# Kernel optimization log

Hardware: AMD Instinct MI355X
Metric: run time of the kernel (lower is better)

Reference implementation:

```python
import jax, jax.numpy as jnp
import numpy as np

B, S, D, H, DH = 2, 4096, 768, 12, 64

def setup_inputs() -> dict:
    key = jax.random.key(0)
    kx, kq, kk, kv = jax.random.split(key, 4)
    x = jax.random.normal(kx, (B, S, D), dtype=jnp.float32)
    # per-head Q/K/V projection weights, stacked over heads: [H, d_in, d_out]
    Wq = jax.random.normal(kq, (H, D, DH), dtype=jnp.float32) * 0.02
    Wk = jax.random.normal(kk, (H, D, DH), dtype=jnp.float32) * 0.02
    Wv = jax.random.normal(kv, (H, D, DH), dtype=jnp.float32) * 0.02
    return {"x": x, "Wq": Wq, "Wk": Wk, "Wv": Wv}

def reference(x, Wq, Wk, Wv):
    b, s, _ = x.shape
    # per-head linear projections (qkv_bias=False), batched over heads
    q = jnp.einsum('bsd,hde->bhse', x, Wq)  # [B,H,S,DH]
    k = jnp.einsum('bsd,hde->bhse', x, Wk)
    v = jnp.einsum('bsd,hde->bhse', x, Wv)
    scale = 1.0 / jnp.sqrt(jnp.asarray(q.shape[-1], q.dtype))
    scores = jnp.einsum('bhqe,bhke->bhqk', q, k) * scale  # [B,H,S,S]
    causal_mask = jnp.triu(jnp.ones((s, s), dtype=bool), k=1)
    scores = jnp.where(causal_mask, -jnp.inf, scores)
    attn = jax.nn.softmax(scores, axis=-1)  # dropout p=0 -> identity
    ctx = jnp.einsum('bhqk,bhke->bhqe', attn, v)  # [B,H,S,DH]
    # concat heads on last dim (matches torch.cat of per-head outputs)
    return ctx.transpose(0, 2, 1, 3).reshape(b, s, -1)  # [B,S,H*DH]
```

## Files before the change

### kernel.cpp

```cpp
#include <hip/hip_runtime.h>
#include <hip/hip_bf16.h>
#include <stdint.h>

#define B_  2
#define S_  4096
#define D_  768
#define H_  12
#define DH_ 64
#define BS_ (B_*S_)

typedef __bf16 bf16x8 __attribute__((ext_vector_type(8)));
typedef short  svec8  __attribute__((ext_vector_type(8)));
typedef float  fvec4  __attribute__((ext_vector_type(4)));
typedef int    ivec4  __attribute__((ext_vector_type(4)));
typedef unsigned short ushort_t;

__device__ __forceinline__ ushort_t bfc(float f){
    return __builtin_bit_cast(ushort_t, (__bf16)f);
}

__device__ __forceinline__ unsigned cvt_pk_bf16(float lo, float hi){
    unsigned r;
    asm("v_cvt_pk_bf16_f32 %0, %1, %2" : "=v"(r) : "v"(lo), "v"(hi));
    return r;
}

__device__ __forceinline__ fvec4 mfma16(svec8 a, svec8 b, fvec4 c){
    return __builtin_amdgcn_mfma_f32_16x16x32_bf16(
        __builtin_bit_cast(bf16x8, a), __builtin_bit_cast(bf16x8, b), c, 0, 0, 0);
}

__global__ __launch_bounds__(256) void prep(
    const float* __restrict__ X,
    const float* __restrict__ Wq, const float* __restrict__ Wk, const float* __restrict__ Wv,
    ushort_t* __restrict__ Xb, ushort_t* __restrict__ Wsz)
{
    const int bid = blockIdx.x;
    if (bid < 3072) {
        size_t idx = ((size_t)bid * 256 + threadIdx.x) * 8;
        float4 d0 = *(const float4*)(X + idx);
        float4 d1 = *(const float4*)(X + idx + 4);
        bf16x8 pk;
        pk[0] = (__bf16)d0.x; pk[1] = (__bf16)d0.y;
        pk[2] = (__bf16)d0.z; pk[3] = (__bf16)d0.w;
        pk[4] = (__bf16)d1.x; pk[5] = (__bf16)d1.y;
        pk[6] = (__bf16)d1.z; pk[7] = (__bf16)d1.w;
        *(svec8*)(Xb + idx) = __builtin_bit_cast(svec8, pk);
    } else {
        const int v  = bid - 3072;
        const int wt = v % 3;
        const int hk = v / 3;
        const int h  = hk / 12, kt = hk % 12;
        const float* W  = (wt == 0) ? Wq : (wt == 1) ? Wk : Wv;
        const float* Wh = W + (size_t)h * (D_ * DH_) + (size_t)kt * 64 * DH_;
        ushort_t* dst = Wsz + (size_t)(hk * 3 + wt) * 4096;
        #pragma unroll
        for (int i = 0; i < 16; i++) {
            int idx = threadIdx.x * 16 + i;
            int k = idx >> 6, n = idx & 63;
            float val = Wh[k * DH_ + n];
            int addr = (((k >> 5) * 4 + (n >> 4)) * 64 + (n & 15) * 4 + ((k >> 3) & 3)) * 8
                     + (k & 7);
            dst[addr] = bfc(val);
        }
    }
}

__global__ __launch_bounds__(256, 3) void qkv_proj(
    const ushort_t* __restrict__ Xb, const ushort_t* __restrict__ Wsz,
    ushort_t* __restrict__ Qb, ushort_t* __restrict__ Kb, ushort_t* __restrict__ Vg)
{
    const int m0 = blockIdx.x * 128;
    const int h  = blockIdx.y;

    __shared__ ushort_t smem[128 * 64 + 3 * 4096];
    ushort_t* Xs  = smem;
    ushort_t* Wts = smem + 128 * 64;
    ushort_t* XsT = smem;

    const int tid  = threadIdx.x;
    const int w    = tid >> 6;
    const int lane = tid & 63;
    const int quad = lane >> 4;
    const int l15  = lane & 15;
    const int lp8  = (l15 * 4 + quad) * 8;

    fvec4 acc[3][2][4];
    #pragma unroll
    for (int wt = 0; wt < 3; wt++)
        #pragma unroll
        for (int i = 0; i < 2; i++)
            #pragma unroll
            for (int j = 0; j < 4; j++) acc[wt][i][j] = (fvec4){0.f, 0.f, 0.f, 0.f};

    const ushort_t* xsrc = Xb + (size_t)m0 * D_;
    const ushort_t* wsrc = Wsz + (size_t)(h * 12) * 3 * 4096;

    int xr[4], xdu[4];
    #pragma unroll
    for (int i = 0; i < 4; i++) {
        int v = tid + 256 * i;
        int r = v >> 3, t = v & 7;
        xr[i]  = r * D_ + t * 8;
        xdu[i] = (((r >> 4) * 2 + (t >> 2)) * 64 + (r & 15) * 4 + (t & 3)) * 8;
    }

    svec8 xd[4];
    #pragma unroll
    for (int i = 0; i < 4; i++) xd[i] = *(const svec8*)(xsrc + xr[i]);

    for (int kt = 0; kt < 12; kt++) {
        const ushort_t* wp = wsrc + (size_t)kt * 3 * 4096;
        svec8 wd[6];
        #pragma unroll
        for (int j = 0; j < 6; j++)
            wd[j] = *(const svec8*)(wp + (tid + 256 * j) * 8);
        #pragma unroll
        for (int i = 0; i < 4; i++) *(svec8*)(Xs + xdu[i]) = xd[i];
        #pragma unroll
        for (int j = 0; j < 6; j++) *(svec8*)(Wts + (tid + 256 * j) * 8) = wd[j];
        __syncthreads();

        if (kt < 11) {
            #pragma unroll
            for (int i = 0; i < 4; i++)
                xd[i] = *(const svec8*)(xsrc + xr[i] + (kt + 1) * 64);
        }

        #pragma unroll
        for (int ks = 0; ks < 2; ks++) {
            svec8 a0 = *(const svec8*)(Xs + (4 * w + ks) * 512 + lp8);
            svec8 a1 = *(const svec8*)(Xs + (4 * w + 2 + ks) * 512 + lp8);
            #pragma unroll
            for (int wt = 0; wt < 3; wt++)
                #pragma unroll
                for (int ns = 0; ns < 4; ns++) {
                    svec8 b = *(const svec8*)(Wts + (wt * 8 + ks * 4 + ns) * 512 + lp8);
                    acc[wt][0][ns] = mfma16(a0, b, acc[wt][0][ns]);
                    acc[wt][1][ns] = mfma16(a1, b, acc[wt][1][ns]);
                }
        }
        __syncthreads();
    }

    const float qs = 0.18033688011112042f;
    #pragma unroll
    for (int ms = 0; ms < 2; ms++)
        #pragma unroll
        for (int ns = 0; ns < 4; ns++)
            #pragma unroll
            for (int r = 0; r < 4; r++) {
                int row = m0 + 32 * w + ms * 16 + quad * 4 + r;
                int col = h * DH_ + ns * 16 + l15;
                Qb[(size_t)row * D_ + col] = bfc(acc[0][ms][ns][r] * qs);
                Kb[(size_t)row * D_ + col] = bfc(acc[1][ms][ns][r]);
            }
    #pragma unroll
    for (int ms = 0; ms < 2; ms++)
        #pragma unroll
        for (int ns = 0; ns < 4; ns++)
            #pragma unroll
            for (int r = 0; r < 4; r++) {
                int sl = 32 * w + ms * 16 + quad * 4 + r;
                int e  = ns * 16 + l15;
                XsT[e * 136 + sl] = bfc(acc[2][ms][ns][r]);
            }
    __syncthreads();
    #pragma unroll
    for (int i = 0; i < 4; i++) {
        int v = tid + 256 * i;
        int e = v >> 4, s0 = (v & 15) * 8;
        svec8 d = *(const svec8*)(XsT + e * 136 + s0);
        *(svec8*)(Vg + (size_t)(h * DH_ + e) * BS_ + m0 + s0) = d;
    }
}

__global__ __launch_bounds__(256, 5) void attn(
    const ushort_t* __restrict__ Qb, const ushort_t* __restrict__ Kb,
    const ushort_t* __restrict__ Vg, float* __restrict__ Out)
{
    const int fid = blockIdx.x;
    const int qt  = (S_ / 64 - 1) - fid / (H_ * B_);
    const int r24 = fid % (H_ * B_);
    const int h   = r24 % H_;
    const int b   = r24 / H_;
    const int q0 = qt * 64;

    const int tid  = threadIdx.x;
    const int w    = tid >> 6;
    const int lane = tid & 63;
    const int quad = lane >> 4;
    const int l15  = lane & 15;

    __shared__ ushort_t Ks[64 * 72];
    __shared__ ushort_t Vt[64 * 72];

    const size_t hb = (size_t)b * S_ * D_ + (size_t)h * DH_;
    const ushort_t* Vh = Vg + (size_t)h * DH_ * BS_ + (size_t)b * S_;

    const int sr = tid >> 3;
    const int sc = (tid & 7) * 8;
    const int pr0 = (((sr      >> 2) & 1) << 5) | (((sr      >> 5) & 1) << 4) |
                    (((sr      >> 4) & 1) << 3) | (((sr      >> 3) & 1) << 2) | (sr & 3);
    const int sr1 = sr + 32;
    const int pr1 = (((sr1 >> 2) & 1) << 5) | (((sr1 >> 5) & 1) << 4) |
                    (((sr1 >> 4) & 1) << 3) | (((sr1 >> 3) & 1) << 2) | (sr1 & 3);

    svec8 aq[2];
    {
        const ushort_t* qrow = Qb + hb + (size_t)(q0 + 16 * w + l15) * D_;
        aq[0] = *(const svec8*)(qrow + quad * 8);
        aq[1] = *(const svec8*)(qrow + 32 + quad * 8);
    }

    float m_i = -INFINITY;
    float ls  = 0.f;
    fvec4 acc[4];
    #pragma unroll
    for (int n = 0; n < 4; n++) acc[n] = (fvec4){0.f, 0.f, 0.f, 0.f};

    const ushort_t* kp = Kb + hb + (size_t)sr * D_ + sc;
    const ushort_t* vp = Vh + (size_t)sr * BS_ + sc;

    svec8 kd[2], vd[2];
    kd[0] = *(const svec8*)(kp);
    kd[1] = *(const svec8*)(kp + (size_t)32 * D_);
    vd[0] = *(const svec8*)(vp);
    vd[1] = *(const svec8*)(vp + (size_t)32 * BS_);
    kp += (size_t)64 * D_;
    vp += 64;
    *(svec8*)(Ks + pr0 * 72 + sc) = kd[0];
    *(svec8*)(Ks + pr1 * 72 + sc) = kd[1];
    *(svec8*)(Vt + sr  * 72 + sc) = vd[0];
    *(svec8*)(Vt + sr1 * 72 + sc) = vd[1];

    for (int kt = 0; kt <= qt; ++kt) {
        __syncthreads();

        if (kt < qt) {
            kd[0] = *(const svec8*)(kp);
            kd[1] = *(const svec8*)(kp + (size_t)32 * D_);
            vd[0] = *(const svec8*)(vp);
            vd[1] = *(const svec8*)(vp + (size_t)32 * BS_);
            kp += (size_t)64 * D_;
            vp += 64;
        }

        fvec4 st[4];
        #pragma unroll
        for (int n = 0; n < 4; n++) st[n] = (fvec4){0.f, 0.f, 0.f, 0.f};
        #pragma unroll
        for (int ks = 0; ks < 2; ks++)
            #pragma unroll
            for (int n = 0; n < 4; n++) {
                svec8 ka = *(const svec8*)(Ks + (n * 16 + l15) * 72 + ks * 32 + quad * 8);
                st[n] = mfma16(ka, aq[ks], st[n]);
            }

        if (kt == qt) {
            #pragma unroll
            for (int n = 0; n < 4; n++)
                #pragma unroll
                for (int r = 0; r < 4; r++) {
                    int key = (n & 1) * 32 + quad * 8 + (n >> 1) * 4 + r;
                    int row = 16 * w + l15;
                    if (key > row) st[n][r] = -INFINITY;
                }
        }

        float mxa = fmaxf(fmaxf(st[0][0], st[0][1]), st[0][2]);
        mxa = fmaxf(fmaxf(mxa, st[0][3]), st[1][0]);
        mxa = fmaxf(fmaxf(mxa, st[1][1]), st[1][2]);
        mxa = fmaxf(mxa, st[1][3]);
        float mxb = fmaxf(fmaxf(st[2][0], st[2][1]), st[2][2]);
        mxb = fmaxf(fmaxf(mxb, st[2][3]), st[3][0]);
        mxb = fmaxf(fmaxf(mxb, st[3][1]), st[3][2]);
        mxb = fmaxf(mxb, st[3][3]);
        float mx = fmaxf(mxa, mxb);
        mx = fmaxf(mx, __shfl_xor(mx, 16));
        mx = fmaxf(mx, __shfl_xor(mx, 32));

        if (__any(mx > m_i)) {
            float mn = fmaxf(m_i, mx);
            float alpha = exp2f(m_i - mn);
            m_i = mn;
            ls *= alpha;
            float ar[4];
            #pragma unroll
            for (int r = 0; r < 4; r++)
                ar[r] = __shfl(alpha, quad * 16 + quad * 4 + r);
            #pragma unroll
            for (int n = 0; n < 4; n++)
                #pragma unroll
                for (int r = 0; r < 4; r++) acc[n][r] *= ar[r];
        }

        ivec4 ai0, ai1;
        float psum[4];
        #pragma unroll
        for (int n = 0; n < 4; n++) {
            float p0 = exp2f(st[n][0] - m_i);
            float p1 = exp2f(st[n][1] - m_i);
            float p2 = exp2f(st[n][2] - m_i);
            float p3 = exp2f(st[n][3] - m_i);
            psum[n] = (p0 + p1) + (p2 + p3);
            unsigned d0 = cvt_pk_bf16(p0, p1);
            unsigned d1 = cvt_pk_bf16(p2, p3);
            if (n == 0)      { ai0[0] = (int)d0; ai0[1] = (int)d1; }
            else if (n == 1) { ai1[0] = (int)d0; ai1[1] = (int)d1; }
            else if (n == 2) { ai0[2] = (int)d0; ai0[3] = (int)d1; }
            else             { ai1[2] = (int)d0; ai1[3] = (int)d1; }
        }
        ls += (psum[0] + psum[2]) + (psum[1] + psum[3]);
        svec8 ap0 = __builtin_bit_cast(svec8, ai0);
        svec8 ap1 = __builtin_bit_cast(svec8, ai1);

        #pragma unroll
        for (int ks = 0; ks < 2; ks++) {
            svec8 ap = ks ? ap1 : ap0;
            #pragma unroll
            for (int n = 0; n < 4; n++) {
                svec8 bv = *(const svec8*)(Vt + (n * 16 + l15) * 72 + ks * 32 + quad * 8);
                acc[n] = mfma16(ap, bv, acc[n]);
            }
        }

        __syncthreads();

        if (kt < qt) {
            *(svec8*)(Ks + pr0 * 72 + sc) = kd[0];
            *(svec8*)(Ks + pr1 * 72 + sc) = kd[1];
            *(svec8*)(Vt + sr  * 72 + sc) = vd[0];
            *(svec8*)(Vt + sr1 * 72 + sc) = vd[1];
        }
    }

    float lsum = ls;
    lsum += __shfl_xor(lsum, 16);
    lsum += __shfl_xor(lsum, 32);
    float li[4];
    #pragma unroll
    for (int r = 0; r < 4; r++)
        li[r] = __shfl(lsum, quad * 16 + quad * 4 + r);
    #pragma unroll
    for (int n = 0; n < 4; n++)
        #pragma unroll
        for (int r = 0; r < 4; r++) {
            int row = q0 + 16 * w + quad * 4 + r;
            int col = h * DH_ + n * 16 + l15;
            Out[((size_t)b * S_ + row) * D_ + col] = acc[n][r] / li[r];
        }
}

extern "C" void kernel_launch(void* const* d_in, const int* in_sizes, int n_in,
                              void* d_out, int out_size, void* d_ws, size_t ws_size,
                              hipStream_t stream)
{
    const float* X  = (const float*)d_in[0];
    const float* Wq = (const float*)d_in[1];
    const float* Wk = (const float*)d_in[2];
    const float* Wv = (const float*)d_in[3];

    ushort_t* Qb = (ushort_t*)d_ws;
    ushort_t* Kb = Qb + (size_t)BS_ * D_;
    ushort_t* Vg = Kb + (size_t)BS_ * D_;

    ushort_t* Xb  = (ushort_t*)d_out;
    ushort_t* Wsz = Xb + (size_t)BS_ * D_;
    float* Out = (float*)d_out;

    prep<<<dim3(3072 + 432), dim3(256), 0, stream>>>(X, Wq, Wk, Wv, Xb, Wsz);
    qkv_proj<<<dim3(64, H_), dim3(256), 0, stream>>>(Xb, Wsz, Qb, Kb, Vg);
    attn<<<dim3((S_ / 64) * H_ * B_), dim3(256), 0, stream>>>(Qb, Kb, Vg, Out);
}
```

Measured before the change: 219.4 us.

## Process two query tiles per attention block with balanced causal scheduling

Each attention block now handles 128 query rows as two 64-row sub-tiles that share every K/V tile staged in shared memory. This halves K/V global loads and LDS staging per query row. Blocks are assigned in three rounds with a remapped tile order to balance the triangular causal workload across 768 blocks. Launch bounds drop to 3 waves per SIMD because of the higher register use, and the weight-swizzle prep now writes vectorised 8-element stores. The cost is lower occupancy and wasted work on the diagonal tiles, where half of sub-tile A is fully masked.

```diff
diff --git a/kernel.cpp b/kernel.cpp
--- a/kernel.cpp
+++ b/kernel.cpp
@@ -55,13 +55,17 @@
         const float* Wh = W + (size_t)h * (D_ * DH_) + (size_t)kt * 64 * DH_;
         ushort_t* dst = Wsz + (size_t)(hk * 3 + wt) * 4096;
         #pragma unroll
-        for (int i = 0; i < 16; i++) {
-            int idx = threadIdx.x * 16 + i;
-            int k = idx >> 6, n = idx & 63;
-            float val = Wh[k * DH_ + n];
-            int addr = (((k >> 5) * 4 + (n >> 4)) * 64 + (n & 15) * 4 + ((k >> 3) & 3)) * 8
-                     + (k & 7);
-            dst[addr] = bfc(val);
+        for (int i = 0; i < 2; i++) {
+            int a    = (threadIdx.x + 256 * i) * 8;
+            int k5   = a >> 11;
+            int nblk = (a >> 9) & 3;
+            int n    = nblk * 16 + ((a >> 5) & 15);
+            int q2   = (a >> 3) & 3;
+            int k0   = k5 * 32 + q2 * 8;
+            bf16x8 pk;
+            #pragma unroll
+            for (int j = 0; j < 8; j++) pk[j] = (__bf16)Wh[(k0 + j) * DH_ + n];
+            *(svec8*)(dst + a) = __builtin_bit_cast(svec8, pk);
         }
     }
 }
@@ -175,16 +179,22 @@
     }
 }
 
-__global__ __launch_bounds__(256, 5) void attn(
+__global__ __launch_bounds__(256, 3) void attn(
     const ushort_t* __restrict__ Qb, const ushort_t* __restrict__ Kb,
     const ushort_t* __restrict__ Vg, float* __restrict__ Out)
 {
     const int fid = blockIdx.x;
-    const int qt  = (S_ / 64 - 1) - fid / (H_ * B_);
-    const int r24 = fid % (H_ * B_);
-    const int h   = r24 % H_;
-    const int b   = r24 / H_;
-    const int q0 = qt * 64;
+    const int c   = fid & 255;
+    const int rnd = fid >> 8;
+    const int t   = c & 31;
+    const int u   = c >> 5;
+    const int qtp = (rnd == 0) ? t : (rnd == 1) ? ((t + 16) & 31)
+                                                : (t < 16 ? 30 - 2 * t : 63 - 2 * t);
+    const int hb  = rnd * 8 + u;
+    const int h   = hb % H_;
+    const int b   = hb / H_;
+    const int q0  = qtp * 128;
+    const int qt2 = 2 * qtp + 1;
 
     const int tid  = threadIdx.x;
     const int w    = tid >> 6;
@@ -195,7 +205,7 @@
     __shared__ ushort_t Ks[64 * 72];
     __shared__ ushort_t Vt[64 * 72];
 
-    const size_t hb = (size_t)b * S_ * D_ + (size_t)h * DH_;
+    const size_t hboff = (size_t)b * S_ * D_ + (size_t)h * DH_;
     const ushort_t* Vh = Vg + (size_t)h * DH_ * BS_ + (size_t)b * S_;
 
     const int sr = tid >> 3;
@@ -206,20 +216,26 @@
     const int pr1 = (((sr1 >> 2) & 1) << 5) | (((sr1 >> 5) & 1) << 4) |
                     (((sr1 >> 4) & 1) << 3) | (((sr1 >> 3) & 1) << 2) | (sr1 & 3);
 
-    svec8 aq[2];
+    svec8 aqA[2], aqB[2];
     {
-        const ushort_t* qrow = Qb + hb + (size_t)(q0 + 16 * w + l15) * D_;
-        aq[0] = *(const svec8*)(qrow + quad * 8);
-        aq[1] = *(const svec8*)(qrow + 32 + quad * 8);
-    }
-
-    float m_i = -INFINITY;
-    float ls  = 0.f;
-    fvec4 acc[4];
-    #pragma unroll
-    for (int n = 0; n < 4; n++) acc[n] = (fvec4){0.f, 0.f, 0.f, 0.f};
-
-    const ushort_t* kp = Kb + hb + (size_t)sr * D_ + sc;
+        const ushort_t* qra = Qb + hboff + (size_t)(q0 + 16 * w + l15) * D_;
+        aqA[0] = *(const svec8*)(qra + quad * 8);
+        aqA[1] = *(const svec8*)(qra + 32 + quad * 8);
+        const ushort_t* qrb = qra + (size_t)64 * D_;
+        aqB[0] = *(const svec8*)(qrb + quad * 8);
+        aqB[1] = *(const svec8*)(qrb + 32 + quad * 8);
+    }
+
+    float miA = -INFINITY, miB = -INFINITY;
+    float lsA = 0.f, lsB = 0.f;
+    fvec4 accA[4], accB[4];
+    #pragma unroll
+    for (int n = 0; n < 4; n++) {
+        accA[n] = (fvec4){0.f, 0.f, 0.f, 0.f};
+        accB[n] = (fvec4){0.f, 0.f, 0.f, 0.f};
+    }
+
+    const ushort_t* kp = Kb + hboff + (size_t)sr * D_ + sc;
     const ushort_t* vp = Vh + (size_t)sr * BS_ + sc;
 
     svec8 kd[2], vd[2];
@@ -234,10 +250,10 @@
     *(svec8*)(Vt + sr  * 72 + sc) = vd[0];
     *(svec8*)(Vt + sr1 * 72 + sc) = vd[1];
 
-    for (int kt = 0; kt <= qt; ++kt) {
+    for (int kt = 0; kt <= qt2; ++kt) {
         __syncthreads();
 
-        if (kt < qt) {
+        if (kt < qt2) {
             kd[0] = *(const svec8*)(kp);
             kd[1] = *(const svec8*)(kp + (size_t)32 * D_);
             vd[0] = *(const svec8*)(vp);
@@ -246,88 +262,147 @@
             vp += 64;
         }
 
-        fvec4 st[4];
-        #pragma unroll
-        for (int n = 0; n < 4; n++) st[n] = (fvec4){0.f, 0.f, 0.f, 0.f};
+        fvec4 stA[4], stB[4];
+        #pragma unroll
+        for (int n = 0; n < 4; n++) {
+            stA[n] = (fvec4){0.f, 0.f, 0.f, 0.f};
+            stB[n] = (fvec4){0.f, 0.f, 0.f, 0.f};
+        }
         #pragma unroll
         for (int ks = 0; ks < 2; ks++)
             #pragma unroll
             for (int n = 0; n < 4; n++) {
                 svec8 ka = *(const svec8*)(Ks + (n * 16 + l15) * 72 + ks * 32 + quad * 8);
-                st[n] = mfma16(ka, aq[ks], st[n]);
-            }
-
-        if (kt == qt) {
+                stA[n] = mfma16(ka, aqA[ks], stA[n]);
+                stB[n] = mfma16(ka, aqB[ks], stB[n]);
+            }
+
+        if (kt == qt2 - 1) {
             #pragma unroll
             for (int n = 0; n < 4; n++)
                 #pragma unroll
                 for (int r = 0; r < 4; r++) {
                     int key = (n & 1) * 32 + quad * 8 + (n >> 1) * 4 + r;
                     int row = 16 * w + l15;
-                    if (key > row) st[n][r] = -INFINITY;
+                    if (key > row) stA[n][r] = -INFINITY;
                 }
         }
-
-        float mxa = fmaxf(fmaxf(st[0][0], st[0][1]), st[0][2]);
-        mxa = fmaxf(fmaxf(mxa, st[0][3]), st[1][0]);
-        mxa = fmaxf(fmaxf(mxa, st[1][1]), st[1][2]);
-        mxa = fmaxf(mxa, st[1][3]);
-        float mxb = fmaxf(fmaxf(st[2][0], st[2][1]), st[2][2]);
-        mxb = fmaxf(fmaxf(mxb, st[2][3]), st[3][0]);
-        mxb = fmaxf(fmaxf(mxb, st[3][1]), st[3][2]);
-        mxb = fmaxf(mxb, st[3][3]);
-        float mx = fmaxf(mxa, mxb);
-        mx = fmaxf(mx, __shfl_xor(mx, 16));
-        mx = fmaxf(mx, __shfl_xor(mx, 32));
-
-        if (__any(mx > m_i)) {
-            float mn = fmaxf(m_i, mx);
-            float alpha = exp2f(m_i - mn);
-            m_i = mn;
-            ls *= alpha;
-            float ar[4];
-            #pragma unroll
-            for (int r = 0; r < 4; r++)
-                ar[r] = __shfl(alpha, quad * 16 + quad * 4 + r);
+        if (kt == qt2) {
             #pragma unroll
             for (int n = 0; n < 4; n++)
                 #pragma unroll
-                for (int r = 0; r < 4; r++) acc[n][r] *= ar[r];
-        }
-
-        ivec4 ai0, ai1;
-        float psum[4];
-        #pragma unroll
-        for (int n = 0; n < 4; n++) {
-            float p0 = exp2f(st[n][0] - m_i);
-            float p1 = exp2f(st[n][1] - m_i);
-            float p2 = exp2f(st[n][2] - m_i);
-            float p3 = exp2f(st[n][3] - m_i);
-            psum[n] = (p0 + p1) + (p2 + p3);
-            unsigned d0 = cvt_pk_bf16(p0, p1);
-            unsigned d1 = cvt_pk_bf16(p2, p3);
-            if (n == 0)      { ai0[0] = (int)d0; ai0[1] = (int)d1; }
-            else if (n == 1) { ai1[0] = (int)d0; ai1[1] = (int)d1; }
-            else if (n == 2) { ai0[2] = (int)d0; ai0[3] = (int)d1; }
-            else             { ai1[2] = (int)d0; ai1[3] = (int)d1; }
-        }
-        ls += (psum[0] + psum[2]) + (psum[1] + psum[3]);
-        svec8 ap0 = __builtin_bit_cast(svec8, ai0);
-        svec8 ap1 = __builtin_bit_cast(svec8, ai1);
+                for (int r = 0; r < 4; r++) {
+                    stA[n][r] = -INFINITY;
+                    int key = (n & 1) * 32 + quad * 8 + (n >> 1) * 4 + r;
+                    int row = 16 * w + l15;
+                    if (key > row) stB[n][r] = -INFINITY;
+                }
+        }
+
+        float mxA, mxB;
+        {
+            float m1 = fmaxf(fmaxf(stA[0][0], stA[0][1]), stA[0][2]);
+            m1 = fmaxf(fmaxf(m1, stA[0][3]), stA[1][0]);
+            m1 = fmaxf(fmaxf(m1, stA[1][1]), stA[1][2]);
+            m1 = fmaxf(m1, stA[1][3]);
+            float m2 = fmaxf(fmaxf(stA[2][0], stA[2][1]), stA[2][2]);
+            m2 = fmaxf(fmaxf(m2, stA[2][3]), stA[3][0]);
+            m2 = fmaxf(fmaxf(m2, stA[3][1]), stA[3][2]);
+            m2 = fmaxf(m2, stA[3][3]);
+            mxA = fmaxf(m1, m2);
+            mxA = fmaxf(mxA, __shfl_xor(mxA, 16));
+            mxA = fmaxf(mxA, __shfl_xor(mxA, 32));
+        }
+        {
+            float m1 = fmaxf(fmaxf(stB[0][0], stB[0][1]), stB[0][2]);
+            m1 = fmaxf(fmaxf(m1, stB[0][3]), stB[1][0]);
+            m1 = fmaxf(fmaxf(m1, stB[1][1]), stB[1][2]);
+            m1 = fmaxf(m1, stB[1][3]);
+            float m2 = fmaxf(fmaxf(stB[2][0], stB[2][1]), stB[2][2]);
+            m2 = fmaxf(fmaxf(m2, stB[2][3]), stB[3][0]);
+            m2 = fmaxf(fmaxf(m2, stB[3][1]), stB[3][2]);
+            m2 = fmaxf(m2, stB[3][3]);
+            mxB = fmaxf(m1, m2);
+            mxB = fmaxf(mxB, __shfl_xor(mxB, 16));
+            mxB = fmaxf(mxB, __shfl_xor(mxB, 32));
+        }
+
+        if (__any((mxA > miA) || (mxB > miB))) {
+            float mnA = fmaxf(miA, mxA), mnB = fmaxf(miB, mxB);
+            float aA = exp2f(miA - mnA), aB = exp2f(miB - mnB);
+            miA = mnA; miB = mnB;
+            lsA *= aA; lsB *= aB;
+            #pragma unroll
+            for (int r = 0; r < 4; r++) {
+                float arA = __shfl(aA, quad * 16 + quad * 4 + r);
+                float arB = __shfl(aB, quad * 16 + quad * 4 + r);
+                #pragma unroll
+                for (int n = 0; n < 4; n++) {
+                    accA[n][r] *= arA;
+                    accB[n][r] *= arB;
+                }
+            }
+        }
+
+        svec8 apA0, apA1, apB0, apB1;
+        {
+            ivec4 ai0, ai1;
+            float ps[4];
+            #pragma unroll
+            for (int n = 0; n < 4; n++) {
+                float p0 = exp2f(stA[n][0] - miA);
+                float p1 = exp2f(stA[n][1] - miA);
+                float p2 = exp2f(stA[n][2] - miA);
+                float p3 = exp2f(stA[n][3] - miA);
+                ps[n] = (p0 + p1) + (p2 + p3);
+                unsigned d0 = cvt_pk_bf16(p0, p1);
+                unsigned d1 = cvt_pk_bf16(p2, p3);
+                if (n == 0)      { ai0[0] = (int)d0; ai0[1] = (int)d1; }
+                else if (n == 1) { ai1[0] = (int)d0; ai1[1] = (int)d1; }
+                else if (n == 2) { ai0[2] = (int)d0; ai0[3] = (int)d1; }
+                else             { ai1[2] = (int)d0; ai1[3] = (int)d1; }
+            }
+            lsA += (ps[0] + ps[2]) + (ps[1] + ps[3]);
+            apA0 = __builtin_bit_cast(svec8, ai0);
+            apA1 = __builtin_bit_cast(svec8, ai1);
+        }
+        {
+            ivec4 ai0, ai1;
+            float ps[4];
+            #pragma unroll
+            for (int n = 0; n < 4; n++) {
+                float p0 = exp2f(stB[n][0] - miB);
+                float p1 = exp2f(stB[n][1] - miB);
+                float p2 = exp2f(stB[n][2] - miB);
+                float p3 = exp2f(stB[n][3] - miB);
+                ps[n] = (p0 + p1) + (p2 + p3);
+                unsigned d0 = cvt_pk_bf16(p0, p1);
+                unsigned d1 = cvt_pk_bf16(p2, p3);
+                if (n == 0)      { ai0[0] = (int)d0; ai0[1] = (int)d1; }
+                else if (n == 1) { ai1[0] = (int)d0; ai1[1] = (int)d1; }
+                else if (n == 2) { ai0[2] = (int)d0; ai0[3] = (int)d1; }
+                else             { ai1[2] = (int)d0; ai1[3] = (int)d1; }
+            }
+            lsB += (ps[0] + ps[2]) + (ps[1] + ps[3]);
+            apB0 = __builtin_bit_cast(svec8, ai0);
+            apB1 = __builtin_bit_cast(svec8, ai1);
+        }
 
         #pragma unroll
         for (int ks = 0; ks < 2; ks++) {
-            svec8 ap = ks ? ap1 : ap0;
+            svec8 apa = ks ? apA1 : apA0;
+            svec8 apb = ks ? apB1 : apB0;
             #pragma unroll
             for (int n = 0; n < 4; n++) {
                 svec8 bv = *(const svec8*)(Vt + (n * 16 + l15) * 72 + ks * 32 + quad * 8);
-                acc[n] = mfma16(ap, bv, acc[n]);
+                accA[n] = mfma16(apa, bv, accA[n]);
+                accB[n] = mfma16(apb, bv, accB[n]);
             }
         }
 
         __syncthreads();
 
-        if (kt < qt) {
+        if (kt < qt2) {
             *(svec8*)(Ks + pr0 * 72 + sc) = kd[0];
             *(svec8*)(Ks + pr1 * 72 + sc) = kd[1];
             *(svec8*)(Vt + sr  * 72 + sc) = vd[0];
@@ -335,21 +410,24 @@
         }
     }
 
-    float lsum = ls;
-    lsum += __shfl_xor(lsum, 16);
-    lsum += __shfl_xor(lsum, 32);
-    float li[4];
-    #pragma unroll
-    for (int r = 0; r < 4; r++)
-        li[r] = __shfl(lsum, quad * 16 + quad * 4 + r);
-    #pragma unroll
-    for (int n = 0; n < 4; n++)
-        #pragma unroll
-        for (int r = 0; r < 4; r++) {
-            int row = q0 + 16 * w + quad * 4 + r;
+    float lsumA = lsA;
+    lsumA += __shfl_xor(lsumA, 16);
+    lsumA += __shfl_xor(lsumA, 32);
+    float lsumB = lsB;
+    lsumB += __shfl_xor(lsumB, 16);
+    lsumB += __shfl_xor(lsumB, 32);
+    #pragma unroll
+    for (int r = 0; r < 4; r++) {
+        float liA = __shfl(lsumA, quad * 16 + quad * 4 + r);
+        float liB = __shfl(lsumB, quad * 16 + quad * 4 + r);
+        int rowA = q0 + 16 * w + quad * 4 + r;
+        #pragma unroll
+        for (int n = 0; n < 4; n++) {
             int col = h * DH_ + n * 16 + l15;
-            Out[((size_t)b * S_ + row) * D_ + col] = acc[n][r] / li[r];
-        }
+            Out[((size_t)b * S_ + rowA) * D_ + col]      = accA[n][r] / liA;
+            Out[((size_t)b * S_ + rowA + 64) * D_ + col] = accB[n][r] / liB;
+        }
+    }
 }
 
 extern "C" void kernel_launch(void* const* d_in, const int* in_sizes, int n_in,
@@ -371,5 +449,5 @@
 
     prep<<<dim3(3072 + 432), dim3(256), 0, stream>>>(X, Wq, Wk, Wv, Xb, Wsz);
     qkv_proj<<<dim3(64, H_), dim3(256), 0, stream>>>(Xb, Wsz, Qb, Kb, Vg);
-    attn<<<dim3((S_ / 64) * H_ * B_), dim3(256), 0, stream>>>(Qb, Kb, Vg, Out);
-}
+    attn<<<dim3(768), dim3(256), 0, stream>>>(Qb, Kb, Vg, Out);
+}
```

Measured after the change: 248.6 us. 1.13x slower.
